# Kernel tuning notes

Measured on AMD Instinct MI355X. Metric: run time of the kernel, lower is better.

The kernel has to match this reference:

```python
import jax, jax.numpy as jnp
import numpy as np

B, S, S_ENC, HID, H = 2, 2048, 2048, 768, 12
D = HID // H  # 64
EPS = 1e-12
MASK_PROB = 0.15


def layer_norm(x, g, b):
    mu = jnp.mean(x, axis=-1, keepdims=True)
    var = jnp.var(x, axis=-1, keepdims=True)
    return (x - mu) * jax.lax.rsqrt(var + EPS) * g + b


def setup_inputs() -> dict:
    key = jax.random.key(0)
    ks = jax.random.split(key, 10)
    inp = {
        "query_hidden_states": jax.random.normal(ks[0], (B, S, HID), jnp.float32),
        "key_value_hidden_states": jax.random.normal(ks[1], (B, S, HID), jnp.float32),
        "encoder_output": jax.random.normal(ks[2], (B, S_ENC, HID), jnp.float32),
        "attention_mask": jnp.ones((B, S), dtype=bool),
        # deterministic stand-in for torch.rand(...) >= mask_prob
        "decoding_mask": jax.random.uniform(ks[3], (B, S, S)) >= MASK_PROB,
        "Wq_w": jax.random.normal(ks[4], (HID, HID), jnp.float32) * 0.02,
        "Wq_b": jnp.zeros((HID,), jnp.float32),
        "Wkv_w": jax.random.normal(ks[5], (2 * HID, HID), jnp.float32) * 0.02,
        "Wkv_b": jnp.zeros((2 * HID,), jnp.float32),
        "dense_w": jax.random.normal(ks[6], (HID, HID), jnp.float32) * 0.02,
        "dense_b": jnp.zeros((HID,), jnp.float32),
        "norm_g": jnp.ones((HID,), jnp.float32),
        "norm_b": jnp.zeros((HID,), jnp.float32),
    }
    return inp


def reference(query_hidden_states, key_value_hidden_states, encoder_output,
              attention_mask, decoding_mask,
              Wq_w, Wq_b, Wkv_w, Wkv_b, dense_w, dense_b, norm_g, norm_b):
    # pre-norm
    q_hs = layer_norm(query_hidden_states, norm_g, norm_b)
    kv_hs = layer_norm(key_value_hidden_states, norm_g, norm_b)

    # kv projection over [encoder_output ; kv_hidden]  -> length L = S_ENC + S
    ekv = jnp.concatenate([encoder_output, kv_hs], axis=1)
    kv = ekv @ Wkv_w.T + Wkv_b                      # [B, L, 2*H*D]
    L = ekv.shape[1]
    kv = kv.reshape(B, L, 2, H, D).transpose(2, 0, 3, 1, 4)  # t b h l d
    k, v = kv[0], kv[1]

    # faithful to source: Wq output is computed but DISCARDED; the raw
    # (pre-normed) hidden states are reshaped into the query.
    _unused_q = q_hs @ Wq_w.T + Wq_b
    query = q_hs.reshape(B, S, H, D).transpose(0, 2, 1, 3)   # b h s d

    # build enhanced decoding mask
    diag = ~jnp.eye(S, dtype=bool)                           # [S, S]
    m = attention_mask[:, None, :] & decoding_mask & diag    # [B, S, S]
    full_mask = jnp.concatenate(
        [jnp.ones((B, S, S_ENC), dtype=bool), m], axis=-1)   # [B, S, L]

    scores = jnp.einsum("bhsd,bhld->bhsl", query, k) / np.sqrt(D).astype(np.float32)
    scores = jnp.where(full_mask[:, None], scores, jnp.finfo(scores.dtype).min)
    attn = jax.nn.softmax(scores, axis=-1)
    out = jnp.einsum("bhsl,bhld->bhsd", attn, v)             # b h s d
    out = out.transpose(0, 2, 1, 3).reshape(B, S, HID)       # b s (h d)

    out = out @ dense_w.T + dense_b
    # dropout is identity (p=0 / eval); residual adds the PRE-NORMED query
    # hidden states (variable was reassigned in the source)
    return out + q_hs
```

## Files before the change

kernel.cpp:

```cpp
#include <hip/hip_runtime.h>
#include <float.h>

constexpr int kB = 2, kS = 2048, kSE = 2048, kL = 4096, kHID = 768, kH = 12, kD = 64;

typedef __attribute__((ext_vector_type(8))) short bfrag;
typedef __attribute__((ext_vector_type(4))) float f32x4;

__device__ __forceinline__ short f2bf(float x) {
  unsigned u = __float_as_uint(x);
  u += 0x7fffu + ((u >> 16) & 1u);
  return (short)(u >> 16);
}

__global__ __launch_bounds__(256) void ln_copy_kernel(
    const float* __restrict__ qin, const float* __restrict__ kvin,
    const float* __restrict__ enc, const float* __restrict__ g,
    const float* __restrict__ beta, float* __restrict__ q_hs,
    short* __restrict__ ekv, short* __restrict__ qbf)
{
  const int row = blockIdx.x;
  const int mode = blockIdx.y;
  const int t = threadIdx.x;
  const int b = row >> 11, s = row & 2047;

  if (mode == 2) {
    const float4* src = (const float4*)(enc + (size_t)row * kHID);
    short* dst = ekv + ((size_t)b * kL + s) * kHID;
    if (t < 192) {
      float4 v = src[t];
      short4 o = {f2bf(v.x), f2bf(v.y), f2bf(v.z), f2bf(v.w)};
      *(short4*)(dst + t * 4) = o;
    }
    return;
  }

  const float* x = (mode == 0 ? qin : kvin) + (size_t)row * kHID;
  float v0 = x[t], v1 = x[t + 256], v2 = x[t + 512];
  float sum = v0 + v1 + v2;
  float sq  = v0 * v0 + v1 * v1 + v2 * v2;
  #pragma unroll
  for (int off = 32; off > 0; off >>= 1) {
    sum += __shfl_down(sum, off, 64);
    sq  += __shfl_down(sq,  off, 64);
  }
  __shared__ float red[8];
  const int wave = t >> 6;
  if ((t & 63) == 0) { red[wave] = sum; red[wave + 4] = sq; }
  __syncthreads();
  const float tsum = red[0] + red[1] + red[2] + red[3];
  const float tsq  = red[4] + red[5] + red[6] + red[7];
  const float mu   = tsum * (1.0f / kHID);
  const float var  = tsq * (1.0f / kHID) - mu * mu;
  const float rstd = rsqrtf(var + 1e-12f);

  const float o0 = (v0 - mu) * rstd * g[t]       + beta[t];
  const float o1 = (v1 - mu) * rstd * g[t + 256] + beta[t + 256];
  const float o2 = (v2 - mu) * rstd * g[t + 512] + beta[t + 512];

  if (mode == 0) {
    float* out = q_hs + (size_t)row * kHID;
    out[t] = o0; out[t + 256] = o1; out[t + 512] = o2;
    short* ob = qbf + (size_t)row * kHID;
    ob[t] = f2bf(o0); ob[t + 256] = f2bf(o1); ob[t + 512] = f2bf(o2);
  } else {
    short* out = ekv + ((size_t)b * kL + kSE + s) * kHID;
    out[t] = f2bf(o0); out[t + 256] = f2bf(o1); out[t + 512] = f2bf(o2);
  }
}

__global__ __launch_bounds__(64) void mask_pack_kernel(
    const unsigned char* __restrict__ am, const unsigned char* __restrict__ dm,
    unsigned long long* __restrict__ pmask)
{
  const int row = blockIdx.x;
  const int b = row >> 11, s = row & 2047;
  const int lane = threadIdx.x;
  const unsigned char* dmr = dm + (size_t)row * kS;
  const unsigned char* amr = am + (size_t)b * kS;
  #pragma unroll 4
  for (int w = 0; w < 32; w++) {
    const int le = w * 64 + lane;
    const bool v = amr[le] && dmr[le] && (s != le);
    const unsigned long long word = __ballot(v);
    if (lane == 0) pmask[(size_t)row * 32 + w] = word;
  }
}

__global__ __launch_bounds__(256) void cvt_w_kernel(
    const float* __restrict__ w1, const float* __restrict__ w2,
    short* __restrict__ o1, short* __restrict__ o2)
{
  const int n1 = 2 * kHID * kHID;
  const int n2 = kHID * kHID;
  const int tot = (n1 + n2) / 4;
  for (int idx = blockIdx.x * 256 + threadIdx.x; idx < tot; idx += gridDim.x * 256) {
    const int i4 = idx * 4;
    if (i4 < n1) {
      float4 v = *(const float4*)(w1 + i4);
      short4 o = {f2bf(v.x), f2bf(v.y), f2bf(v.z), f2bf(v.w)};
      *(short4*)(o1 + i4) = o;
    } else {
      float4 v = *(const float4*)(w2 + (i4 - n1));
      short4 o = {f2bf(v.x), f2bf(v.y), f2bf(v.z), f2bf(v.w)};
      *(short4*)(o2 + (i4 - n1)) = o;
    }
  }
}

template <int MODE>
__global__ __launch_bounds__(256) void gemm_mfma(
    const short* __restrict__ A, const short* __restrict__ W,
    const float* __restrict__ bias, short* __restrict__ kb,
    short* __restrict__ vt, float* __restrict__ outf,
    const float* __restrict__ resid)
{
  __shared__ short As[128 * 64];
  __shared__ short Bs[128 * 64];
  const int t = threadIdx.x;
  const int m0 = blockIdx.x * 128;
  const int n0 = blockIdx.y * 128 + (MODE == 1 ? kHID : 0);
  const int wv = t >> 6, lane = t & 63;
  const int g = lane >> 4, ln = lane & 15;
  const int wr = wv >> 1, wc = wv & 1;

  f32x4 acc[4][4] = {};

  for (int kt = 0; kt < kHID; kt += 64) {
    uint4 ra[4], rb[4];
    #pragma unroll
    for (int r = 0; r < 4; r++) {
      const int f = t + r * 256;
      const int row = f >> 3, c = f & 7;
      ra[r] = *(const uint4*)(A + (size_t)(m0 + row) * kHID + kt + c * 8);
      rb[r] = *(const uint4*)(W + (size_t)(n0 + row) * kHID + kt + c * 8);
    }
    __syncthreads();
    #pragma unroll
    for (int r = 0; r < 4; r++) {
      const int f = t + r * 256;
      const int row = f >> 3, c = f & 7;
      const int sc = c ^ (row & 7);
      *(uint4*)&As[row * 64 + sc * 8] = ra[r];
      *(uint4*)&Bs[row * 64 + sc * 8] = rb[r];
    }
    __syncthreads();

    bfrag a0[4], a1[4], b0[4], b1[4];
    #pragma unroll
    for (int i = 0; i < 4; i++) {
      const int ar = wr * 64 + i * 16 + ln;
      a0[i] = *(const bfrag*)&As[ar * 64 + (((g + 0) ^ (ln & 7)) << 3)];
      a1[i] = *(const bfrag*)&As[ar * 64 + (((g + 4) ^ (ln & 7)) << 3)];
      const int br = wc * 64 + i * 16 + ln;
      b0[i] = *(const bfrag*)&Bs[br * 64 + (((g + 0) ^ (ln & 7)) << 3)];
      b1[i] = *(const bfrag*)&Bs[br * 64 + (((g + 4) ^ (ln & 7)) << 3)];
    }
    #pragma unroll
    for (int i = 0; i < 4; i++)
      #pragma unroll
      for (int j = 0; j < 4; j++) {
        if (MODE == 1) {
          acc[i][j] = __builtin_amdgcn_mfma_f32_16x16x32_bf16(b0[i], a0[j], acc[i][j], 0, 0, 0);
          acc[i][j] = __builtin_amdgcn_mfma_f32_16x16x32_bf16(b1[i], a1[j], acc[i][j], 0, 0, 0);
        } else {
          acc[i][j] = __builtin_amdgcn_mfma_f32_16x16x32_bf16(a0[i], b0[j], acc[i][j], 0, 0, 0);
          acc[i][j] = __builtin_amdgcn_mfma_f32_16x16x32_bf16(a1[i], b1[j], acc[i][j], 0, 0, 0);
        }
      }
  }

  if (MODE == 0) {
    #pragma unroll
    for (int j = 0; j < 4; j++) {
      const int n = n0 + wc * 64 + j * 16 + ln;
      const float bn = bias[n];
      const int h = n >> 6, d = n & 63;
      #pragma unroll
      for (int i = 0; i < 4; i++)
        #pragma unroll
        for (int r = 0; r < 4; r++) {
          const int m = m0 + wr * 64 + i * 16 + g * 4 + r;
          kb[(((size_t)((m >> 12) * kH + h)) * kL + (m & 4095)) * kD + d] =
              f2bf(acc[i][j][r] + bn);
        }
    }
  } else if (MODE == 1) {
    #pragma unroll
    for (int i = 0; i < 4; i++)
      #pragma unroll
      for (int r = 0; r < 4; r++) {
        const int n = n0 + wc * 64 + i * 16 + g * 4 + r;
        const float bn = bias[n];
        const int nn = n - kHID;
        const int h = nn >> 6, d = nn & 63;
        #pragma unroll
        for (int j = 0; j < 4; j++) {
          const int m = m0 + wr * 64 + j * 16 + ln;
          vt[(((size_t)((m >> 12) * kH + h)) * kD + d) * kL + (m & 4095)] =
              f2bf(acc[i][j][r] + bn);
        }
      }
  } else {
    #pragma unroll
    for (int j = 0; j < 4; j++) {
      const int n = n0 + wc * 64 + j * 16 + ln;
      const float bn = bias[n];
      #pragma unroll
      for (int i = 0; i < 4; i++)
        #pragma unroll
        for (int r = 0; r < 4; r++) {
          const int m = m0 + wr * 64 + i * 16 + g * 4 + r;
          const size_t off = (size_t)m * kHID + n;
          outf[off] = acc[i][j][r] + bn + resid[off];
        }
    }
  }
}

__global__ __launch_bounds__(256) void attn_mfma(
    const short* __restrict__ qbf, const short* __restrict__ kbuf,
    const short* __restrict__ vtbuf, const unsigned long long* __restrict__ pmask,
    short* __restrict__ attn_out)
{
  __shared__ short Ks[64 * 64];
  __shared__ short Vs[64 * 64];
  __shared__ short Ps[4][16 * 64];

  const int qt = blockIdx.x, h = blockIdx.y, b = blockIdx.z;
  const int s0 = qt * 64;
  const int t = threadIdx.x;
  const int wv = t >> 6, lane = t & 63;
  const int g = lane >> 4, ln = lane & 15;
  const float scale = 0.125f;

  const short* Kg = kbuf + ((size_t)(b * kH + h)) * kL * kD;
  const short* Vg = vtbuf + ((size_t)(b * kH + h)) * kD * kL;

  const short* qrow = qbf + ((size_t)(b * kS + s0 + wv * 16 + ln)) * kHID + h * kD;
  const bfrag aQ0 = *(const bfrag*)(qrow + g * 8);
  const bfrag aQ1 = *(const bfrag*)(qrow + 32 + g * 8);

  const int srow = t >> 2, sc4 = t & 3;
  const int c0 = sc4 * 2, c1 = c0 + 1;
  const int swz0 = srow * 64 + ((c0 ^ (srow & 7)) << 3);
  const int swz1 = srow * 64 + ((c1 ^ (srow & 7)) << 3);

  f32x4 accO[4] = {};
  float mrun[4] = {-FLT_MAX, -FLT_MAX, -FLT_MAX, -FLT_MAX};
  float lrun[4] = {0.f, 0.f, 0.f, 0.f};
  const f32x4 zero = {0.f, 0.f, 0.f, 0.f};

  for (int lt = 0; lt < kL / 64; lt++) {
    __syncthreads();
    {
      const short* kgp = Kg + ((size_t)(lt * 64 + srow)) * kD + sc4 * 16;
      uint4 ka = *(const uint4*)kgp;
      uint4 kb2 = *(const uint4*)(kgp + 8);
      *(uint4*)&Ks[swz0] = ka;
      *(uint4*)&Ks[swz1] = kb2;
      const short* vgp = Vg + (size_t)srow * kL + lt * 64 + sc4 * 16;
      uint4 va = *(const uint4*)vgp;
      uint4 vb = *(const uint4*)(vgp + 8);
      *(uint4*)&Vs[swz0] = va;
      *(uint4*)&Vs[swz1] = vb;
    }
    __syncthreads();

    f32x4 accS[4];
    #pragma unroll
    for (int nt = 0; nt < 4; nt++) {
      const int row = nt * 16 + ln;
      const bfrag bK0 = *(const bfrag*)&Ks[row * 64 + (((g + 0) ^ (ln & 7)) << 3)];
      const bfrag bK1 = *(const bfrag*)&Ks[row * 64 + (((g + 4) ^ (ln & 7)) << 3)];
      accS[nt] = __builtin_amdgcn_mfma_f32_16x16x32_bf16(aQ0, bK0, zero, 0, 0, 0);
      accS[nt] = __builtin_amdgcn_mfma_f32_16x16x32_bf16(aQ1, bK1, accS[nt], 0, 0, 0);
    }

    if (lt >= kSE / 64) {
      #pragma unroll
      for (int r = 0; r < 4; r++) {
        const int q = s0 + wv * 16 + g * 4 + r;
        const unsigned long long wmask =
            pmask[((size_t)(b * kS + q)) * 32 + (lt - kSE / 64)];
        #pragma unroll
        for (int nt = 0; nt < 4; nt++) {
          const bool valid = (wmask >> (nt * 16 + ln)) & 1ull;
          accS[nt][r] = valid ? accS[nt][r] * scale : -FLT_MAX;
        }
      }
    } else {
      #pragma unroll
      for (int nt = 0; nt < 4; nt++)
        #pragma unroll
        for (int r = 0; r < 4; r++) accS[nt][r] *= scale;
    }

    float corr[4];
    #pragma unroll
    for (int r = 0; r < 4; r++) {
      float tm = fmaxf(fmaxf(accS[0][r], accS[1][r]), fmaxf(accS[2][r], accS[3][r]));
      #pragma unroll
      for (int mk = 1; mk < 16; mk <<= 1) tm = fmaxf(tm, __shfl_xor(tm, mk, 64));
      const float mn = fmaxf(mrun[r], tm);
      corr[r] = __expf(mrun[r] - mn);
      mrun[r] = mn;
      float ps = 0.f;
      #pragma unroll
      for (int nt = 0; nt < 4; nt++) {
        const float p = __expf(accS[nt][r] - mn);
        accS[nt][r] = p;
        ps += p;
      }
      #pragma unroll
      for (int mk = 1; mk < 16; mk <<= 1) ps += __shfl_xor(ps, mk, 64);
      lrun[r] = lrun[r] * corr[r] + ps;
      const int prow = g * 4 + r;
      #pragma unroll
      for (int nt = 0; nt < 4; nt++) {
        const int l = nt * 16 + ln;
        Ps[wv][prow * 64 + (((l >> 3) ^ (prow & 7)) << 3) + (l & 7)] = f2bf(accS[nt][r]);
      }
    }

    #pragma unroll
    for (int nt = 0; nt < 4; nt++) {
      f32x4 a = accO[nt];
      a[0] *= corr[0]; a[1] *= corr[1]; a[2] *= corr[2]; a[3] *= corr[3];
      accO[nt] = a;
    }

    const bfrag aP0 = *(const bfrag*)&Ps[wv][ln * 64 + (((g + 0) ^ (ln & 7)) << 3)];
    const bfrag aP1 = *(const bfrag*)&Ps[wv][ln * 64 + (((g + 4) ^ (ln & 7)) << 3)];
    #pragma unroll
    for (int nt = 0; nt < 4; nt++) {
      const int row = nt * 16 + ln;
      const bfrag bV0 = *(const bfrag*)&Vs[row * 64 + (((g + 0) ^ (ln & 7)) << 3)];
      const bfrag bV1 = *(const bfrag*)&Vs[row * 64 + (((g + 4) ^ (ln & 7)) << 3)];
      accO[nt] = __builtin_amdgcn_mfma_f32_16x16x32_bf16(aP0, bV0, accO[nt], 0, 0, 0);
      accO[nt] = __builtin_amdgcn_mfma_f32_16x16x32_bf16(aP1, bV1, accO[nt], 0, 0, 0);
    }
  }

  float inv[4];
  #pragma unroll
  for (int r = 0; r < 4; r++) inv[r] = 1.0f / lrun[r];
  #pragma unroll
  for (int nt = 0; nt < 4; nt++)
    #pragma unroll
    for (int r = 0; r < 4; r++) {
      const int q = s0 + wv * 16 + g * 4 + r;
      attn_out[((size_t)(b * kS + q)) * kHID + h * kD + nt * 16 + ln] =
          f2bf(accO[nt][r] * inv[r]);
    }
}

extern "C" void kernel_launch(void* const* d_in, const int* in_sizes, int n_in,
                              void* d_out, int out_size, void* d_ws, size_t ws_size,
                              hipStream_t stream) {
  const float* q_in    = (const float*)d_in[0];
  const float* kv_in   = (const float*)d_in[1];
  const float* enc     = (const float*)d_in[2];
  const unsigned char* am = (const unsigned char*)d_in[3];
  const unsigned char* dm = (const unsigned char*)d_in[4];
  const float* wkv_w   = (const float*)d_in[7];
  const float* wkv_b   = (const float*)d_in[8];
  const float* dense_w = (const float*)d_in[9];
  const float* dense_b = (const float*)d_in[10];
  const float* norm_g  = (const float*)d_in[11];
  const float* norm_b  = (const float*)d_in[12];
  float* out = (float*)d_out;

  float* ws = (float*)d_ws;
  float* q_hs   = ws;
  short* ekv    = (short*)(ws + 3145728);
  short* kbuf   = (short*)(ws + 6291456);
  short* vtbuf  = (short*)(ws + 9437184);
  short* qbf    = (short*)(ws + 12582912);
  unsigned long long* pmask = (unsigned long long*)(ws + 14155776);
  short* wkv_bf = (short*)(ws + 14417920);
  short* wd_bf  = (short*)(ws + 15007744);
  short* attn_bf = ekv;

  hipLaunchKernelGGL(ln_copy_kernel, dim3(kB * kS, 3), dim3(256), 0, stream,
                     q_in, kv_in, enc, norm_g, norm_b, q_hs, ekv, qbf);
  hipLaunchKernelGGL(mask_pack_kernel, dim3(kB * kS), dim3(64), 0, stream,
                     am, dm, pmask);
  hipLaunchKernelGGL(cvt_w_kernel, dim3(1024), dim3(256), 0, stream,
                     wkv_w, dense_w, wkv_bf, wd_bf);
  hipLaunchKernelGGL((gemm_mfma<0>), dim3(64, 6), dim3(256), 0, stream,
                     ekv, wkv_bf, wkv_b, kbuf, nullptr, nullptr, nullptr);
  hipLaunchKernelGGL((gemm_mfma<1>), dim3(64, 6), dim3(256), 0, stream,
                     ekv, wkv_bf, wkv_b, nullptr, vtbuf, nullptr, nullptr);
  hipLaunchKernelGGL(attn_mfma, dim3(kS / 64, kH, kB), dim3(256), 0, stream,
                     qbf, kbuf, vtbuf, pmask, attn_bf);
  hipLaunchKernelGGL((gemm_mfma<2>), dim3(32, 6), dim3(256), 0, stream,
                     attn_bf, wd_bf, dense_b, nullptr, nullptr, out, q_hs);
}
```

Measured before the change: 492.7 us.

## Restructure attention to load K/V fragments directly and merge K/V GEMM launches

The attention kernel drops its shared-memory K/V staging and the per-tile block barriers. Each wave now loads K and V^T fragments straight from global memory and computes S transposed, so every lane owns one query row and softmax reductions need only two shuffles. The softmax scale and log2(e) are folded into the bf16 query during layernorm, and exp2f replaces __expf. The rescale is skipped when no row's maximum grows, and occupancy is hinted with launch_bounds(256,3). The K and V projection GEMMs are merged into one launch and f2bf now uses the HIP intrinsic. In exchange, each wave loads K/V from global independently, which means more cache traffic.

```diff
diff --git a/kernel.cpp b/kernel.cpp
--- a/kernel.cpp
+++ b/kernel.cpp
@@ -1,4 +1,5 @@
 #include <hip/hip_runtime.h>
+#include <hip/hip_bf16.h>
 #include <float.h>
 
 constexpr int kB = 2, kS = 2048, kSE = 2048, kL = 4096, kHID = 768, kH = 12, kD = 64;
@@ -7,10 +8,13 @@
 typedef __attribute__((ext_vector_type(4))) float f32x4;
 
 __device__ __forceinline__ short f2bf(float x) {
-  unsigned u = __float_as_uint(x);
-  u += 0x7fffu + ((u >> 16) & 1u);
-  return (short)(u >> 16);
-}
+  __hip_bfloat16 h = __float2bfloat16(x);
+  short s;
+  __builtin_memcpy(&s, &h, 2);
+  return s;
+}
+
+#define QSCALE (0.125f * 1.44269504088896340736f)
 
 __global__ __launch_bounds__(256) void ln_copy_kernel(
     const float* __restrict__ qin, const float* __restrict__ kvin,
@@ -61,7 +65,9 @@
     float* out = q_hs + (size_t)row * kHID;
     out[t] = o0; out[t + 256] = o1; out[t + 512] = o2;
     short* ob = qbf + (size_t)row * kHID;
-    ob[t] = f2bf(o0); ob[t + 256] = f2bf(o1); ob[t + 512] = f2bf(o2);
+    ob[t]       = f2bf(o0 * QSCALE);
+    ob[t + 256] = f2bf(o1 * QSCALE);
+    ob[t + 512] = f2bf(o2 * QSCALE);
   } else {
     short* out = ekv + ((size_t)b * kL + kSE + s) * kHID;
     out[t] = f2bf(o0); out[t + 256] = f2bf(o1); out[t + 512] = f2bf(o2);
@@ -118,7 +124,8 @@
   __shared__ short Bs[128 * 64];
   const int t = threadIdx.x;
   const int m0 = blockIdx.x * 128;
-  const int n0 = blockIdx.y * 128 + (MODE == 1 ? kHID : 0);
+  const int n0 = blockIdx.y * 128;
+  const bool isV = (MODE == 0) && (n0 >= kHID);
   const int wv = t >> 6, lane = t & 63;
   const int g = lane >> 4, ln = lane & 15;
   const int wr = wv >> 1, wc = wv & 1;
@@ -155,21 +162,26 @@
       b0[i] = *(const bfrag*)&Bs[br * 64 + (((g + 0) ^ (ln & 7)) << 3)];
       b1[i] = *(const bfrag*)&Bs[br * 64 + (((g + 4) ^ (ln & 7)) << 3)];
     }
-    #pragma unroll
-    for (int i = 0; i < 4; i++)
-      #pragma unroll
-      for (int j = 0; j < 4; j++) {
-        if (MODE == 1) {
+    if (isV) {
+      #pragma unroll
+      for (int i = 0; i < 4; i++)
+        #pragma unroll
+        for (int j = 0; j < 4; j++) {
           acc[i][j] = __builtin_amdgcn_mfma_f32_16x16x32_bf16(b0[i], a0[j], acc[i][j], 0, 0, 0);
           acc[i][j] = __builtin_amdgcn_mfma_f32_16x16x32_bf16(b1[i], a1[j], acc[i][j], 0, 0, 0);
-        } else {
+        }
+    } else {
+      #pragma unroll
+      for (int i = 0; i < 4; i++)
+        #pragma unroll
+        for (int j = 0; j < 4; j++) {
           acc[i][j] = __builtin_amdgcn_mfma_f32_16x16x32_bf16(a0[i], b0[j], acc[i][j], 0, 0, 0);
           acc[i][j] = __builtin_amdgcn_mfma_f32_16x16x32_bf16(a1[i], b1[j], acc[i][j], 0, 0, 0);
         }
-      }
-  }
-
-  if (MODE == 0) {
+    }
+  }
+
+  if (MODE == 0 && !isV) {
     #pragma unroll
     for (int j = 0; j < 4; j++) {
       const int n = n0 + wc * 64 + j * 16 + ln;
@@ -184,7 +196,7 @@
               f2bf(acc[i][j][r] + bn);
         }
     }
-  } else if (MODE == 1) {
+  } else if (MODE == 0) {
     #pragma unroll
     for (int i = 0; i < 4; i++)
       #pragma unroll
@@ -217,13 +229,11 @@
   }
 }
 
-__global__ __launch_bounds__(256) void attn_mfma(
+__global__ __launch_bounds__(256, 3) void attn_mfma(
     const short* __restrict__ qbf, const short* __restrict__ kbuf,
     const short* __restrict__ vtbuf, const unsigned long long* __restrict__ pmask,
     short* __restrict__ attn_out)
 {
-  __shared__ short Ks[64 * 64];
-  __shared__ short Vs[64 * 64];
   __shared__ short Ps[4][16 * 64];
 
   const int qt = blockIdx.x, h = blockIdx.y, b = blockIdx.z;
@@ -231,126 +241,123 @@
   const int t = threadIdx.x;
   const int wv = t >> 6, lane = t & 63;
   const int g = lane >> 4, ln = lane & 15;
-  const float scale = 0.125f;
 
   const short* Kg = kbuf + ((size_t)(b * kH + h)) * kL * kD;
   const short* Vg = vtbuf + ((size_t)(b * kH + h)) * kD * kL;
 
   const short* qrow = qbf + ((size_t)(b * kS + s0 + wv * 16 + ln)) * kHID + h * kD;
-  const bfrag aQ0 = *(const bfrag*)(qrow + g * 8);
-  const bfrag aQ1 = *(const bfrag*)(qrow + 32 + g * 8);
-
-  const int srow = t >> 2, sc4 = t & 3;
-  const int c0 = sc4 * 2, c1 = c0 + 1;
-  const int swz0 = srow * 64 + ((c0 ^ (srow & 7)) << 3);
-  const int swz1 = srow * 64 + ((c1 ^ (srow & 7)) << 3);
+  const bfrag bQ0 = *(const bfrag*)(qrow + g * 8);
+  const bfrag bQ1 = *(const bfrag*)(qrow + 32 + g * 8);
+
+  const unsigned long long* pmrow =
+      pmask + ((size_t)(b * kS + s0 + wv * 16 + ln)) * 32;
+
+  short* myPs = &Ps[wv][0];
+  const int rdP0 = ln * 64 + (((g + 0) ^ (ln & 7)) << 3);
+  const int rdP1 = ln * 64 + (((g + 4) ^ (ln & 7)) << 3);
 
   f32x4 accO[4] = {};
-  float mrun[4] = {-FLT_MAX, -FLT_MAX, -FLT_MAX, -FLT_MAX};
-  float lrun[4] = {0.f, 0.f, 0.f, 0.f};
+  float mrun = -FLT_MAX, lrun = 0.f;
   const f32x4 zero = {0.f, 0.f, 0.f, 0.f};
 
   for (int lt = 0; lt < kL / 64; lt++) {
-    __syncthreads();
-    {
-      const short* kgp = Kg + ((size_t)(lt * 64 + srow)) * kD + sc4 * 16;
-      uint4 ka = *(const uint4*)kgp;
-      uint4 kb2 = *(const uint4*)(kgp + 8);
-      *(uint4*)&Ks[swz0] = ka;
-      *(uint4*)&Ks[swz1] = kb2;
-      const short* vgp = Vg + (size_t)srow * kL + lt * 64 + sc4 * 16;
-      uint4 va = *(const uint4*)vgp;
-      uint4 vb = *(const uint4*)(vgp + 8);
-      *(uint4*)&Vs[swz0] = va;
-      *(uint4*)&Vs[swz1] = vb;
-    }
-    __syncthreads();
+    bfrag aK0[4], aK1[4], bV0[4], bV1[4];
+    #pragma unroll
+    for (int nt = 0; nt < 4; nt++) {
+      const short* kp = Kg + (size_t)(lt * 64 + nt * 16 + ln) * kD;
+      aK0[nt] = *(const bfrag*)(kp + g * 8);
+      aK1[nt] = *(const bfrag*)(kp + 32 + g * 8);
+    }
+    #pragma unroll
+    for (int nt = 0; nt < 4; nt++) {
+      const short* vp = Vg + (size_t)(nt * 16 + ln) * kL + lt * 64;
+      bV0[nt] = *(const bfrag*)(vp + g * 8);
+      bV1[nt] = *(const bfrag*)(vp + 32 + g * 8);
+    }
 
     f32x4 accS[4];
     #pragma unroll
     for (int nt = 0; nt < 4; nt++) {
-      const int row = nt * 16 + ln;
-      const bfrag bK0 = *(const bfrag*)&Ks[row * 64 + (((g + 0) ^ (ln & 7)) << 3)];
-      const bfrag bK1 = *(const bfrag*)&Ks[row * 64 + (((g + 4) ^ (ln & 7)) << 3)];
-      accS[nt] = __builtin_amdgcn_mfma_f32_16x16x32_bf16(aQ0, bK0, zero, 0, 0, 0);
-      accS[nt] = __builtin_amdgcn_mfma_f32_16x16x32_bf16(aQ1, bK1, accS[nt], 0, 0, 0);
+      accS[nt] = __builtin_amdgcn_mfma_f32_16x16x32_bf16(aK0[nt], bQ0, zero, 0, 0, 0);
+      accS[nt] = __builtin_amdgcn_mfma_f32_16x16x32_bf16(aK1[nt], bQ1, accS[nt], 0, 0, 0);
     }
 
     if (lt >= kSE / 64) {
+      const unsigned long long wm = pmrow[lt - kSE / 64];
+      #pragma unroll
+      for (int nt = 0; nt < 4; nt++) {
+        const unsigned nib = (unsigned)(wm >> (nt * 16 + g * 4)) & 0xFu;
+        #pragma unroll
+        for (int r = 0; r < 4; r++)
+          if (!((nib >> r) & 1u)) accS[nt][r] = -FLT_MAX;
+      }
+    }
+
+    float pmax = accS[0][0];
+    #pragma unroll
+    for (int nt = 0; nt < 4; nt++)
+      #pragma unroll
+      for (int r = 0; r < 4; r++) pmax = fmaxf(pmax, accS[nt][r]);
+    pmax = fmaxf(pmax, __shfl_xor(pmax, 16, 64));
+    pmax = fmaxf(pmax, __shfl_xor(pmax, 32, 64));
+
+    if (!__all(pmax <= mrun)) {
+      const float mn = fmaxf(mrun, pmax);
+      const float corr = exp2f(mrun - mn);
+      mrun = mn;
+      lrun *= corr;
+      float c4[4];
+      #pragma unroll
+      for (int r = 0; r < 4; r++) c4[r] = __shfl(corr, g * 4 + r, 64);
+      #pragma unroll
+      for (int nt = 0; nt < 4; nt++) {
+        accO[nt][0] *= c4[0]; accO[nt][1] *= c4[1];
+        accO[nt][2] *= c4[2]; accO[nt][3] *= c4[3];
+      }
+    }
+
+    float ps = 0.f;
+    #pragma unroll
+    for (int nt = 0; nt < 4; nt++)
       #pragma unroll
       for (int r = 0; r < 4; r++) {
-        const int q = s0 + wv * 16 + g * 4 + r;
-        const unsigned long long wmask =
-            pmask[((size_t)(b * kS + q)) * 32 + (lt - kSE / 64)];
-        #pragma unroll
-        for (int nt = 0; nt < 4; nt++) {
-          const bool valid = (wmask >> (nt * 16 + ln)) & 1ull;
-          accS[nt][r] = valid ? accS[nt][r] * scale : -FLT_MAX;
-        }
-      }
-    } else {
-      #pragma unroll
-      for (int nt = 0; nt < 4; nt++)
-        #pragma unroll
-        for (int r = 0; r < 4; r++) accS[nt][r] *= scale;
-    }
-
-    float corr[4];
-    #pragma unroll
-    for (int r = 0; r < 4; r++) {
-      float tm = fmaxf(fmaxf(accS[0][r], accS[1][r]), fmaxf(accS[2][r], accS[3][r]));
-      #pragma unroll
-      for (int mk = 1; mk < 16; mk <<= 1) tm = fmaxf(tm, __shfl_xor(tm, mk, 64));
-      const float mn = fmaxf(mrun[r], tm);
-      corr[r] = __expf(mrun[r] - mn);
-      mrun[r] = mn;
-      float ps = 0.f;
-      #pragma unroll
-      for (int nt = 0; nt < 4; nt++) {
-        const float p = __expf(accS[nt][r] - mn);
+        const float p = exp2f(accS[nt][r] - mrun);
         accS[nt][r] = p;
         ps += p;
       }
-      #pragma unroll
-      for (int mk = 1; mk < 16; mk <<= 1) ps += __shfl_xor(ps, mk, 64);
-      lrun[r] = lrun[r] * corr[r] + ps;
-      const int prow = g * 4 + r;
-      #pragma unroll
-      for (int nt = 0; nt < 4; nt++) {
-        const int l = nt * 16 + ln;
-        Ps[wv][prow * 64 + (((l >> 3) ^ (prow & 7)) << 3) + (l & 7)] = f2bf(accS[nt][r]);
-      }
-    }
+    ps += __shfl_xor(ps, 16, 64);
+    ps += __shfl_xor(ps, 32, 64);
+    lrun += ps;
 
     #pragma unroll
     for (int nt = 0; nt < 4; nt++) {
-      f32x4 a = accO[nt];
-      a[0] *= corr[0]; a[1] *= corr[1]; a[2] *= corr[2]; a[3] *= corr[3];
-      accO[nt] = a;
-    }
-
-    const bfrag aP0 = *(const bfrag*)&Ps[wv][ln * 64 + (((g + 0) ^ (ln & 7)) << 3)];
-    const bfrag aP1 = *(const bfrag*)&Ps[wv][ln * 64 + (((g + 4) ^ (ln & 7)) << 3)];
+      short4 p4 = {f2bf(accS[nt][0]), f2bf(accS[nt][1]),
+                   f2bf(accS[nt][2]), f2bf(accS[nt][3])};
+      const int chunk = nt * 2 + (g >> 1);
+      const int sc = chunk ^ (ln & 7);
+      *(short4*)&myPs[ln * 64 + sc * 8 + (g & 1) * 4] = p4;
+    }
+
+    const bfrag aP0 = *(const bfrag*)&myPs[rdP0];
+    const bfrag aP1 = *(const bfrag*)&myPs[rdP1];
     #pragma unroll
     for (int nt = 0; nt < 4; nt++) {
-      const int row = nt * 16 + ln;
-      const bfrag bV0 = *(const bfrag*)&Vs[row * 64 + (((g + 0) ^ (ln & 7)) << 3)];
-      const bfrag bV1 = *(const bfrag*)&Vs[row * 64 + (((g + 4) ^ (ln & 7)) << 3)];
-      accO[nt] = __builtin_amdgcn_mfma_f32_16x16x32_bf16(aP0, bV0, accO[nt], 0, 0, 0);
-      accO[nt] = __builtin_amdgcn_mfma_f32_16x16x32_bf16(aP1, bV1, accO[nt], 0, 0, 0);
-    }
-  }
-
-  float inv[4];
+      accO[nt] = __builtin_amdgcn_mfma_f32_16x16x32_bf16(aP0, bV0[nt], accO[nt], 0, 0, 0);
+      accO[nt] = __builtin_amdgcn_mfma_f32_16x16x32_bf16(aP1, bV1[nt], accO[nt], 0, 0, 0);
+    }
+  }
+
+  const float linv = 1.0f / lrun;
+  float i4[4];
   #pragma unroll
-  for (int r = 0; r < 4; r++) inv[r] = 1.0f / lrun[r];
+  for (int r = 0; r < 4; r++) i4[r] = __shfl(linv, g * 4 + r, 64);
   #pragma unroll
   for (int nt = 0; nt < 4; nt++)
     #pragma unroll
     for (int r = 0; r < 4; r++) {
       const int q = s0 + wv * 16 + g * 4 + r;
       attn_out[((size_t)(b * kS + q)) * kHID + h * kD + nt * 16 + ln] =
-          f2bf(accO[nt][r] * inv[r]);
+          f2bf(accO[nt][r] * i4[r]);
     }
 }
 
@@ -387,12 +394,10 @@
                      am, dm, pmask);
   hipLaunchKernelGGL(cvt_w_kernel, dim3(1024), dim3(256), 0, stream,
                      wkv_w, dense_w, wkv_bf, wd_bf);
-  hipLaunchKernelGGL((gemm_mfma<0>), dim3(64, 6), dim3(256), 0, stream,
-                     ekv, wkv_bf, wkv_b, kbuf, nullptr, nullptr, nullptr);
-  hipLaunchKernelGGL((gemm_mfma<1>), dim3(64, 6), dim3(256), 0, stream,
-                     ekv, wkv_bf, wkv_b, nullptr, vtbuf, nullptr, nullptr);
+  hipLaunchKernelGGL((gemm_mfma<0>), dim3(64, 12), dim3(256), 0, stream,
+                     ekv, wkv_bf, wkv_b, kbuf, vtbuf, nullptr, nullptr);
   hipLaunchKernelGGL(attn_mfma, dim3(kS / 64, kH, kB), dim3(256), 0, stream,
                      qbf, kbuf, vtbuf, pmask, attn_bf);
-  hipLaunchKernelGGL((gemm_mfma<2>), dim3(32, 6), dim3(256), 0, stream,
+  hipLaunchKernelGGL((gemm_mfma<1>), dim3(32, 6), dim3(256), 0, stream,
                      attn_bf, wd_bf, dense_b, nullptr, nullptr, out, q_hs);
 }
```

After: 654.3 us. +32.8%, slower.
